# Performance work log

Measured on AMD Instinct MI355X. Metric: run time of the kernel, lower is better.

The kernel has to match this reference:

```python
import jax, jax.numpy as jnp
import numpy as np

HIDDEN = 2048
N_HEADS = 16
HEAD_DIM = 128
N_KV_HEADS = 4
MAX_POS = 4096
NEG_INF = -1e9


def _fixed_pos_embedding(features, length):
    # matches generate_fixed_pos_embedding: freqs over arange(0, features, 2)/features
    fraction = jnp.arange(0, features, 2, dtype=jnp.float32) / features
    timescale = 10000.0 ** fraction
    inv_freq = 1.0 / timescale
    sinusoid = jnp.einsum('i,j->ij', jnp.arange(length, dtype=jnp.float32), inv_freq)
    sinusoid = jnp.concatenate([sinusoid, sinusoid], axis=-1)  # [length, features]
    return jnp.sin(sinusoid), jnp.cos(sinusoid)


def setup_inputs() -> dict:
    key = jax.random.key(0)
    k0, k1, k2, k3, k4 = jax.random.split(key, 5)
    B, S = 2, 2048
    hidden_states = jax.random.normal(k0, (B, S, HIDDEN), dtype=jnp.float32)
    # causal additive mask [B,1,S,S]; module forces mask[:, :, :, 0] = 0
    causal = jnp.where(jnp.tril(jnp.ones((S, S), dtype=bool)), 0.0, NEG_INF).astype(jnp.float32)
    causal = causal.at[:, 0].set(0.0)
    attention_mask = jnp.broadcast_to(causal[None, None], (B, 1, S, S))
    std = 0.02
    q_w = jax.random.normal(k1, (N_HEADS * HEAD_DIM, HIDDEN), dtype=jnp.float32) * std
    k_w = jax.random.normal(k2, (N_KV_HEADS * HEAD_DIM, HIDDEN), dtype=jnp.float32) * std
    v_w = jax.random.normal(k3, (N_KV_HEADS * HEAD_DIM, HIDDEN), dtype=jnp.float32) * std
    o_w = jax.random.normal(k4, (HIDDEN, N_HEADS * HEAD_DIM), dtype=jnp.float32) * std
    sin, cos = _fixed_pos_embedding(HEAD_DIM, MAX_POS)
    return {"hidden_states": hidden_states, "attention_mask": attention_mask,
            "q_w": q_w, "k_w": k_w, "v_w": v_w, "o_w": o_w, "sin": sin, "cos": cos}


def _rotate_half(x):
    d = x.shape[-1] // 2
    return jnp.concatenate([-x[..., d:], x[..., :d]], axis=-1)


def reference(hidden_states, attention_mask, q_w, k_w, v_w, o_w, sin, cos):
    B, S, _ = hidden_states.shape
    D = cos.shape[-1]
    H = q_w.shape[0] // D
    KV = k_w.shape[0] // D
    n_rep = H // KV

    # QKV projections (nn.Linear: y = x @ W^T), split into heads: [B,S,h,D]
    q = jnp.einsum('bsh,oh->bso', hidden_states, q_w).reshape(B, S, H, D)
    k = jnp.einsum('bsh,oh->bso', hidden_states, k_w).reshape(B, S, KV, D)
    v = jnp.einsum('bsh,oh->bso', hidden_states, v_w).reshape(B, S, KV, D)

    # rotary embedding (non-decode path: q and k share cos/sin[:S])
    c = cos[:S][None, :, None, :]
    s = sin[:S][None, :, None, :]
    q = q * c + _rotate_half(q) * s
    k = k * c + _rotate_half(k) * s

    # repeat_kv (repeat_interleave along head dim) for GQA
    k = jnp.repeat(k, n_rep, axis=2)  # [B,S,H,D]
    v = jnp.repeat(v, n_rep, axis=2)

    # NOTE: no 1/sqrt(D) scaling -- module uses softmax_scale=1.0
    scores = jnp.einsum('bqhd,bkhd->bhqk', q, k) + attention_mask
    weights = jax.nn.softmax(scores.astype(jnp.float32), axis=-1).astype(q.dtype)
    attn = jnp.einsum('bhqk,bkhd->bqhd', weights, v).reshape(B, S, H * D)
    return jnp.einsum('bso,ho->bsh', attn, o_w)
```

## Files before the change

kernel.cpp:

```cpp
#include <hip/hip_runtime.h>

typedef __bf16 bf16x8 __attribute__((ext_vector_type(8)));
typedef float f32x4 __attribute__((ext_vector_type(4)));

#define LOG2E 1.44269504088896340736f

#define GLDS16(g, l) __builtin_amdgcn_global_load_lds(                         \
    (const __attribute__((address_space(1))) unsigned int*)(g),                \
    (__attribute__((address_space(3))) unsigned int*)(l), 16, 0, 0)

__global__ __launch_bounds__(256) void split_matrix(
    const float* __restrict__ src, __bf16* __restrict__ dh, __bf16* __restrict__ dl)
{
    const size_t t = (size_t)(blockIdx.x * 256 + threadIdx.x) * 8;
    float4 a = *(const float4*)(src + t);
    float4 b = *(const float4*)(src + t + 4);
    float f[8] = {a.x, a.y, a.z, a.w, b.x, b.y, b.z, b.w};
    bf16x8 h, l;
#pragma unroll
    for (int i = 0; i < 8; ++i) {
        __bf16 hh = (__bf16)f[i];
        h[i] = hh; l[i] = (__bf16)(f[i] - (float)hh);
    }
    *(bf16x8*)(dh + t) = h;
    *(bf16x8*)(dl + t) = l;
}

__global__ __launch_bounds__(256) void gemm_planes(
    const __bf16* __restrict__ Ah, const __bf16* __restrict__ Al,
    const __bf16* __restrict__ Bh, const __bf16* __restrict__ Bl,
    float* __restrict__ C, int K, int ldc)
{
    __shared__ __bf16 sAh[128 * 32], sAl[128 * 32];
    __shared__ __bf16 sBh[128 * 32], sBl[128 * 32];

    const int tid  = threadIdx.x;
    const int lane = tid & 63;
    const int wave = tid >> 6;
    const int m0 = blockIdx.y * 128;
    const int n0 = blockIdx.x * 128;

    const int sr  = wave * 32 + (lane >> 2);
    const int sc  = (lane & 3) * 8;
    const __bf16* ga0 = Ah + (size_t)(m0 + sr) * K + sc;
    const __bf16* ga1 = ga0 + (size_t)16 * K;
    const __bf16* gA0 = Al + (size_t)(m0 + sr) * K + sc;
    const __bf16* gA1 = gA0 + (size_t)16 * K;
    const __bf16* gb0 = Bh + (size_t)(n0 + sr) * K + sc;
    const __bf16* gb1 = gb0 + (size_t)16 * K;
    const __bf16* gB0 = Bl + (size_t)(n0 + sr) * K + sc;
    const __bf16* gB1 = gB0 + (size_t)16 * K;
    __bf16* la0 = &sAh[(wave * 32) * 32];
    __bf16* la1 = &sAh[(wave * 32 + 16) * 32];
    __bf16* lA0 = &sAl[(wave * 32) * 32];
    __bf16* lA1 = &sAl[(wave * 32 + 16) * 32];
    __bf16* lb0 = &sBh[(wave * 32) * 32];
    __bf16* lb1 = &sBh[(wave * 32 + 16) * 32];
    __bf16* lB0 = &sBl[(wave * 32) * 32];
    __bf16* lB1 = &sBl[(wave * 32 + 16) * 32];

    f32x4 acc[4][4];
    for (int mi = 0; mi < 4; ++mi)
        for (int ni = 0; ni < 4; ++ni)
            acc[mi][ni] = (f32x4){0.f, 0.f, 0.f, 0.f};

    const int wm = (wave & 1) * 64;
    const int wn = (wave >> 1) * 64;
    const int fr = lane & 15;
    const int fc = (lane >> 4) * 8;
    const int dr = (lane >> 4) * 4;

    for (int k0 = 0; k0 < K; k0 += 32) {
        GLDS16(ga0, la0); GLDS16(ga1, la1);
        GLDS16(gA0, lA0); GLDS16(gA1, lA1);
        GLDS16(gb0, lb0); GLDS16(gb1, lb1);
        GLDS16(gB0, lB0); GLDS16(gB1, lB1);
        ga0 += 32; ga1 += 32; gA0 += 32; gA1 += 32;
        gb0 += 32; gb1 += 32; gB0 += 32; gB1 += 32;
        __syncthreads();

        bf16x8 afh[4], afl[4], bfh[4], bfl[4];
#pragma unroll
        for (int i = 0; i < 4; ++i) {
            afh[i] = *(const bf16x8*)&sAh[(wm + i * 16 + fr) * 32 + fc];
            afl[i] = *(const bf16x8*)&sAl[(wm + i * 16 + fr) * 32 + fc];
            bfh[i] = *(const bf16x8*)&sBh[(wn + i * 16 + fr) * 32 + fc];
            bfl[i] = *(const bf16x8*)&sBl[(wn + i * 16 + fr) * 32 + fc];
        }
#pragma unroll
        for (int mi = 0; mi < 4; ++mi)
#pragma unroll
            for (int ni = 0; ni < 4; ++ni) {
                acc[mi][ni] = __builtin_amdgcn_mfma_f32_16x16x32_bf16(
                    afh[mi], bfh[ni], acc[mi][ni], 0, 0, 0);
                acc[mi][ni] = __builtin_amdgcn_mfma_f32_16x16x32_bf16(
                    afl[mi], bfh[ni], acc[mi][ni], 0, 0, 0);
                acc[mi][ni] = __builtin_amdgcn_mfma_f32_16x16x32_bf16(
                    afh[mi], bfl[ni], acc[mi][ni], 0, 0, 0);
            }
        __syncthreads();
    }

    for (int mi = 0; mi < 4; ++mi)
        for (int ni = 0; ni < 4; ++ni)
            for (int r = 0; r < 4; ++r) {
                int row = m0 + wm + mi * 16 + dr + r;
                int col = n0 + wn + ni * 16 + fr;
                C[(size_t)row * ldc + col] = acc[mi][ni][r];
            }
}

__global__ __launch_bounds__(256) void rope_q(
    float* __restrict__ qkv,
    const float* __restrict__ sinp, const float* __restrict__ cosp)
{
    int t = blockIdx.x * 256 + threadIdx.x;
    int row = t >> 10;
    int rem = t & 1023;
    int col = (rem >> 6) * 128 + (rem & 63);
    int s = row & 2047;
    int d = col & 127;

    float* p = qkv + (size_t)row * 3072 + col;
    float x0  = p[0];
    float x1  = p[64];
    float c0  = cosp[s * 128 + d];
    float c1  = cosp[s * 128 + d + 64];
    float sn0 = sinp[s * 128 + d];
    float sn1 = sinp[s * 128 + d + 64];
    p[0]  = x0 * c0 - x1 * sn0;
    p[64] = x1 * c1 + x0 * sn1;
}

__global__ __launch_bounds__(256) void prep_kv(
    const float* __restrict__ qkv,
    const float* __restrict__ sinp, const float* __restrict__ cosp,
    __bf16* __restrict__ ksp, __bf16* __restrict__ vtsp)
{
    __shared__ float vs[32][132];

    const int tid = threadIdx.x;
    const int kb  = blockIdx.x;
    const int kvh = blockIdx.y;
    const int b   = blockIdx.z;

    {
        const int key = tid >> 1;
        const int dh  = (tid & 1) * 32;
        const int pos = kb * 128 + key;
        const int ksw = key & 7;
        const float* src = qkv + (size_t)(b * 2048 + pos) * 3072 + 2048 + kvh * 128;
        __bf16* dst = ksp + ((size_t)((b * 4 + kvh) * 2048) + pos) * 256;
        const float* cp = cosp + pos * 128;
        const float* sp = sinp + pos * 128;
#pragma unroll
        for (int g = 0; g < 4; ++g) {
            int d0 = dh + g * 8;
            float4 x0a = *(const float4*)(src + d0);
            float4 x0b = *(const float4*)(src + d0 + 4);
            float4 x1a = *(const float4*)(src + d0 + 64);
            float4 x1b = *(const float4*)(src + d0 + 68);
            float4 c0a = *(const float4*)(cp + d0);
            float4 c0b = *(const float4*)(cp + d0 + 4);
            float4 c1a = *(const float4*)(cp + d0 + 64);
            float4 c1b = *(const float4*)(cp + d0 + 68);
            float4 s0a = *(const float4*)(sp + d0);
            float4 s0b = *(const float4*)(sp + d0 + 4);
            float4 s1a = *(const float4*)(sp + d0 + 64);
            float4 s1b = *(const float4*)(sp + d0 + 68);
            float x0[8] = {x0a.x,x0a.y,x0a.z,x0a.w,x0b.x,x0b.y,x0b.z,x0b.w};
            float x1[8] = {x1a.x,x1a.y,x1a.z,x1a.w,x1b.x,x1b.y,x1b.z,x1b.w};
            float c0[8] = {c0a.x,c0a.y,c0a.z,c0a.w,c0b.x,c0b.y,c0b.z,c0b.w};
            float c1[8] = {c1a.x,c1a.y,c1a.z,c1a.w,c1b.x,c1b.y,c1b.z,c1b.w};
            float s0[8] = {s0a.x,s0a.y,s0a.z,s0a.w,s0b.x,s0b.y,s0b.z,s0b.w};
            float s1[8] = {s1a.x,s1a.y,s1a.z,s1a.w,s1b.x,s1b.y,s1b.z,s1b.w};
            bf16x8 h0, l0, h1, l1;
#pragma unroll
            for (int i = 0; i < 8; ++i) {
                float y0 = x0[i] * c0[i] - x1[i] * s0[i];
                float y1 = x1[i] * c1[i] + x0[i] * s1[i];
                __bf16 hh0 = (__bf16)y0;
                __bf16 hh1 = (__bf16)y1;
                h0[i] = hh0; l0[i] = (__bf16)(y0 - (float)hh0);
                h1[i] = hh1; l1[i] = (__bf16)(y1 - (float)hh1);
            }
            const int bb = d0 >> 3;
            *(bf16x8*)(dst + ((bb        ^ ksw) << 3)) = h0;
            *(bf16x8*)(dst + (((bb + 8)  ^ ksw) << 3)) = h1;
            *(bf16x8*)(dst + (((bb + 16) ^ ksw) << 3)) = l0;
            *(bf16x8*)(dst + (((bb + 24) ^ ksw) << 3)) = l1;
        }
    }

    for (int st = 0; st < 4; ++st) {
        __syncthreads();
        {
            const int key = tid >> 3;
            const int dc  = (tid & 7) * 16;
            const float* vsrc = qkv + (size_t)(b * 2048 + kb * 128 + st * 32 + key) * 3072
                                + 2560 + kvh * 128 + dc;
            float4 v0 = *(const float4*)(vsrc);
            float4 v1 = *(const float4*)(vsrc + 4);
            float4 v2 = *(const float4*)(vsrc + 8);
            float4 v3 = *(const float4*)(vsrc + 12);
            *(float4*)&vs[key][dc]      = v0;
            *(float4*)&vs[key][dc + 4]  = v1;
            *(float4*)&vs[key][dc + 8]  = v2;
            *(float4*)&vs[key][dc + 12] = v3;
        }
        __syncthreads();
        {
            const int plane = tid >> 7;
            const int d     = tid & 127;
            bf16x8 ob[4];
#pragma unroll
            for (int k = 0; k < 32; ++k) {
                float x = vs[k][d];
                __bf16 hh = (__bf16)x;
                ob[k >> 3][k & 7] = plane ? (__bf16)(x - (float)hh) : hh;
            }
            const int rV  = plane * 128 + d;
            const int vsw = (d >> 1) & 3;
            __bf16* dst = vtsp + ((size_t)((b * 4 + kvh) * 64 + kb * 4 + st)) * 8192
                               + (size_t)rV * 32;
            *(bf16x8*)(dst + ((0 ^ vsw) << 3)) = ob[0];
            *(bf16x8*)(dst + ((1 ^ vsw) << 3)) = ob[1];
            *(bf16x8*)(dst + ((2 ^ vsw) << 3)) = ob[2];
            *(bf16x8*)(dst + ((3 ^ vsw) << 3)) = ob[3];
        }
    }
}

__global__ __launch_bounds__(256, 2) void flash_attn(
    const float* __restrict__ qkv,
    const __bf16* __restrict__ ksp,
    const __bf16* __restrict__ vtsp,
    __bf16* __restrict__ attnh, __bf16* __restrict__ attnl)
{
    __shared__ __bf16 Ks[2][32 * 256];
    __shared__ __bf16 Vt[2][256 * 32];
    __shared__ unsigned int Psf[4][2][512];

    const int tid  = threadIdx.x;
    const int lane = tid & 63;
    const int wave = tid >> 6;
    const int id   = blockIdx.x;
    const int pair = id & 7;
    const int kvh  = pair & 3;
    const int b    = pair >> 2;
    const int u    = id >> 3;
    const int qb   = (u >> 5) ? (u & 31) : 63 - (u & 31);
    const int h    = kvh * 4 + wave;

    const int fr  = lane & 15;
    const int g   = lane >> 4;
    const int fc  = g * 8;
    const int dr  = g * 4;
    const int frs = fr & 7;

    bf16x8 aqh[2][4], aql[2][4];
    for (int rs = 0; rs < 2; ++rs) {
        const size_t qrow = (size_t)(b * 2048 + qb * 32 + rs * 16 + fr) * 3072 + h * 128;
        for (int ks = 0; ks < 4; ++ks) {
            float4 qv[2];
            qv[0] = *(const float4*)(qkv + qrow + ks * 32 + fc);
            qv[1] = *(const float4*)(qkv + qrow + ks * 32 + fc + 4);
            const float* qf = (const float*)qv;
            bf16x8 h8, l8;
#pragma unroll
            for (int i = 0; i < 8; ++i) {
                float x = qf[i];
                __bf16 hh = (__bf16)x;
                h8[i] = hh; l8[i] = (__bf16)(x - (float)hh);
            }
            aqh[rs][ks] = h8; aql[rs][ks] = l8;
        }
    }
    asm volatile("s_waitcnt vmcnt(0)" ::: "memory");
    __builtin_amdgcn_sched_barrier(0);

    bf16x8 ones;
#pragma unroll
    for (int i = 0; i < 8; ++i) ones[i] = (__bf16)1.0f;

    f32x4 o[2][8];
    for (int rs = 0; rs < 2; ++rs)
        for (int dg = 0; dg < 8; ++dg) o[rs][dg] = (f32x4){0.f, 0.f, 0.f, 0.f};
    f32x4 ls[2] = {(f32x4){0.f,0.f,0.f,0.f}, (f32x4){0.f,0.f,0.f,0.f}};

    const int ntiles = qb + 1;
    const __bf16* kg0 = ksp + (size_t)(b * 4 + kvh) * 2048 * 256 + wave * 2048 + lane * 8;
    const __bf16* vg0 = vtsp + (size_t)(b * 4 + kvh) * 64 * 8192 + wave * 2048 + lane * 8;

    {
        __bf16* kl = &Ks[0][wave * 2048];
        __bf16* vl = &Vt[0][wave * 2048];
        GLDS16(kg0,        kl);       GLDS16(kg0 + 512,  kl + 512);
        GLDS16(kg0 + 1024, kl + 1024);GLDS16(kg0 + 1536, kl + 1536);
        GLDS16(vg0,        vl);       GLDS16(vg0 + 512,  vl + 512);
        GLDS16(vg0 + 1024, vl + 1024);GLDS16(vg0 + 1536, vl + 1536);
    }

    for (int kt = 0; kt < ntiles; ++kt) {
        if (kt + 1 < ntiles) {
            const __bf16* kg = kg0 + (size_t)(kt + 1) * 8192;
            const __bf16* vg = vg0 + (size_t)(kt + 1) * 8192;
            __bf16* kl = &Ks[(kt + 1) & 1][wave * 2048];
            __bf16* vl = &Vt[(kt + 1) & 1][wave * 2048];
            GLDS16(kg,        kl);       GLDS16(kg + 512,  kl + 512);
            GLDS16(kg + 1024, kl + 1024);GLDS16(kg + 1536, kl + 1536);
            GLDS16(vg,        vl);       GLDS16(vg + 512,  vl + 512);
            GLDS16(vg + 1024, vl + 1024);GLDS16(vg + 1536, vl + 1536);
            asm volatile("s_waitcnt vmcnt(8)" ::: "memory");
        } else {
            asm volatile("s_waitcnt vmcnt(0)" ::: "memory");
        }
        __builtin_amdgcn_sched_barrier(0);
        __builtin_amdgcn_s_barrier();
        __builtin_amdgcn_sched_barrier(0);

        const int buf = kt & 1;
        const int k0 = kt * 32;

        f32x4 s[2][2];
        s[0][0] = s[0][1] = s[1][0] = s[1][1] = (f32x4){0.f, 0.f, 0.f, 0.f};
        __builtin_amdgcn_s_setprio(1);
#pragma unroll
        for (int ks = 0; ks < 4; ++ks) {
            const int bh = ks * 4 + g;
            bf16x8 b0h = *(const bf16x8*)&Ks[buf][fr * 256        + ((bh        ^ frs) << 3)];
            bf16x8 b0l = *(const bf16x8*)&Ks[buf][fr * 256        + (((bh + 16) ^ frs) << 3)];
            bf16x8 b1h = *(const bf16x8*)&Ks[buf][(16 + fr) * 256 + ((bh        ^ frs) << 3)];
            bf16x8 b1l = *(const bf16x8*)&Ks[buf][(16 + fr) * 256 + (((bh + 16) ^ frs) << 3)];
#pragma unroll
            for (int rs = 0; rs < 2; ++rs) {
                s[rs][0] = __builtin_amdgcn_mfma_f32_16x16x32_bf16(aqh[rs][ks], b0h, s[rs][0], 0, 0, 0);
                s[rs][0] = __builtin_amdgcn_mfma_f32_16x16x32_bf16(aql[rs][ks], b0h, s[rs][0], 0, 0, 0);
                s[rs][0] = __builtin_amdgcn_mfma_f32_16x16x32_bf16(aqh[rs][ks], b0l, s[rs][0], 0, 0, 0);
                s[rs][1] = __builtin_amdgcn_mfma_f32_16x16x32_bf16(aqh[rs][ks], b1h, s[rs][1], 0, 0, 0);
                s[rs][1] = __builtin_amdgcn_mfma_f32_16x16x32_bf16(aql[rs][ks], b1h, s[rs][1], 0, 0, 0);
                s[rs][1] = __builtin_amdgcn_mfma_f32_16x16x32_bf16(aqh[rs][ks], b1l, s[rs][1], 0, 0, 0);
            }
        }
        __builtin_amdgcn_s_setprio(0);

        const bool diag = (kt == ntiles - 1);
#pragma unroll
        for (int rs = 0; rs < 2; ++rs) {
            f32x4 s0 = s[rs][0], s1 = s[rs][1];
            if (diag) {
#pragma unroll
                for (int r = 0; r < 4; ++r) {
                    const int qg = qb * 32 + rs * 16 + dr + r;
                    if (k0 + fr > qg)      s0[r] = -1e30f;
                    if (k0 + 16 + fr > qg) s1[r] = -1e30f;
                }
            }
            uint4 w0, w1;
#pragma unroll
            for (int r = 0; r < 4; ++r) {
                float x0 = exp2f(s0[r] * LOG2E);
                float x1 = exp2f(s1[r] * LOG2E);
                __bf16 h0 = (__bf16)x0;
                __bf16 h1 = (__bf16)x1;
                unsigned u0 = ((unsigned)__builtin_bit_cast(unsigned short, h0) << 16)
                            |  (unsigned)__builtin_bit_cast(unsigned short, (__bf16)(x0 - (float)h0));
                unsigned u1 = ((unsigned)__builtin_bit_cast(unsigned short, h1) << 16)
                            |  (unsigned)__builtin_bit_cast(unsigned short, (__bf16)(x1 - (float)h1));
                ((unsigned*)&w0)[r] = u0;
                ((unsigned*)&w1)[r] = u1;
            }
            unsigned int* pw = &Psf[wave][rs][0];
            const int sb = (fr * 4 + g) ^ (((fr >> 3) & 1) << 2);
            *(uint4*)(pw + sb * 4)        = w0;
            *(uint4*)(pw + (sb + 64) * 4) = w1;
        }
        asm volatile("s_waitcnt lgkmcnt(0)" ::: "memory");
        __builtin_amdgcn_sched_barrier(0);

        bf16x8 ph[2], pl[2];
#pragma unroll
        for (int rs = 0; rs < 2; ++rs) {
#pragma unroll
            for (int j = 0; j < 8; ++j) {
                const int col = fc + j;
                const int sR  = (col * 4 + (fr >> 2)) ^ ((g & 1) << 2);
                const unsigned v = Psf[wave][rs][sR * 4 + (fr & 3)];
                ph[rs][j] = __builtin_bit_cast(__bf16, (unsigned short)(v >> 16));
                pl[rs][j] = __builtin_bit_cast(__bf16, (unsigned short)(v & 0xffffu));
            }
        }

        __builtin_amdgcn_s_setprio(1);
        ls[0] = __builtin_amdgcn_mfma_f32_16x16x32_bf16(ph[0], ones, ls[0], 0, 0, 0);
        ls[0] = __builtin_amdgcn_mfma_f32_16x16x32_bf16(pl[0], ones, ls[0], 0, 0, 0);
        ls[1] = __builtin_amdgcn_mfma_f32_16x16x32_bf16(ph[1], ones, ls[1], 0, 0, 0);
        ls[1] = __builtin_amdgcn_mfma_f32_16x16x32_bf16(pl[1], ones, ls[1], 0, 0, 0);
#pragma unroll
        for (int dg = 0; dg < 8; ++dg) {
            const int d0 = dg * 16 + fr;
            const int sw = (g ^ ((d0 >> 1) & 3)) << 3;
            bf16x8 bvh = *(const bf16x8*)&Vt[buf][d0 * 32 + sw];
            bf16x8 bvl = *(const bf16x8*)&Vt[buf][(d0 + 128) * 32 + sw];
#pragma unroll
            for (int rs = 0; rs < 2; ++rs) {
                o[rs][dg] = __builtin_amdgcn_mfma_f32_16x16x32_bf16(ph[rs], bvh, o[rs][dg], 0, 0, 0);
                o[rs][dg] = __builtin_amdgcn_mfma_f32_16x16x32_bf16(pl[rs], bvh, o[rs][dg], 0, 0, 0);
                o[rs][dg] = __builtin_amdgcn_mfma_f32_16x16x32_bf16(ph[rs], bvl, o[rs][dg], 0, 0, 0);
            }
        }
        __builtin_amdgcn_s_setprio(0);

        __builtin_amdgcn_s_barrier();
    }

    for (int rs = 0; rs < 2; ++rs) {
        const size_t orow = (size_t)(b * 2048 + qb * 32 + rs * 16);
        for (int dg = 0; dg < 8; ++dg)
            for (int r = 0; r < 4; ++r) {
                float val = o[rs][dg][r] / ls[rs][r];
                size_t idx = (orow + dr + r) * 2048 + h * 128 + dg * 16 + fr;
                __bf16 hh = (__bf16)val;
                attnh[idx] = hh;
                attnl[idx] = (__bf16)(val - (float)hh);
            }
    }
}

extern "C" void kernel_launch(void* const* d_in, const int* in_sizes, int n_in,
                              void* d_out, int out_size, void* d_ws, size_t ws_size,
                              hipStream_t stream)
{
    const float* hs   = (const float*)d_in[0];
    const float* qw   = (const float*)d_in[2];
    const float* kw   = (const float*)d_in[3];
    const float* vw   = (const float*)d_in[4];
    const float* ow   = (const float*)d_in[5];
    const float* sinp = (const float*)d_in[6];
    const float* cosp = (const float*)d_in[7];
    float* outp = (float*)d_out;

    char* w = (char*)d_ws;
    float*  qkv  = (float*)w;   w += (size_t)4096 * 3072 * 4;
    __bf16* ksp  = (__bf16*)w;  w += (size_t)8 * 2048 * 256 * 2;
    __bf16* vtsp = (__bf16*)w;  w += (size_t)8 * 64 * 8192 * 2;
    __bf16* wqh  = (__bf16*)w;  w += (size_t)3072 * 2048 * 2;
    __bf16* wql  = (__bf16*)w;  w += (size_t)3072 * 2048 * 2;
    __bf16* owh  = (__bf16*)w;  w += (size_t)2048 * 2048 * 2;
    __bf16* owl  = (__bf16*)w;  w += (size_t)2048 * 2048 * 2;
    __bf16* hsh  = (__bf16*)w;  w += (size_t)4096 * 2048 * 2;
    __bf16* hsl  = (__bf16*)w;  w += (size_t)4096 * 2048 * 2;
    __bf16* attnh = hsh;
    __bf16* attnl = hsl;

    split_matrix<<<4096, 256, 0, stream>>>(hs, hsh, hsl);
    split_matrix<<<2048, 256, 0, stream>>>(qw, wqh, wql);
    split_matrix<<<512,  256, 0, stream>>>(kw, wqh + (size_t)2048 * 2048,
                                               wql + (size_t)2048 * 2048);
    split_matrix<<<512,  256, 0, stream>>>(vw, wqh + (size_t)2560 * 2048,
                                               wql + (size_t)2560 * 2048);
    split_matrix<<<2048, 256, 0, stream>>>(ow, owh, owl);

    gemm_planes<<<dim3(24, 32), 256, 0, stream>>>(hsh, hsl, wqh, wql, qkv, 2048, 3072);
    rope_q<<<16384, 256, 0, stream>>>(qkv, sinp, cosp);
    prep_kv<<<dim3(16, 4, 2), 256, 0, stream>>>(qkv, sinp, cosp, ksp, vtsp);
    flash_attn<<<512, 256, 0, stream>>>(qkv, ksp, vtsp, attnh, attnl);
    gemm_planes<<<dim3(16, 32), 256, 0, stream>>>(attnh, attnl, owh, owl, outp, 2048, 2048);
}
```

Measured before the change: 600.5 us.

## Rewrite split-bf16 GEMM with larger tiles, double buffering and swizzled LDS layout

Replaces the 128x128 single-buffered GEMM with a 512-thread kernel that uses 256xBN tiles (192 for QKV, 128 for output projection), double-buffered LDS staging via global_load_lds and explicit vmcnt waits, and a remapped block order for cache locality. The split and attention-output writers now store bf16 planes in an XOR-swizzled layout so LDS fragment reads avoid bank conflicts. This targets the projection GEMMs' load latency and LDS conflicts. In exchange it adds register pressure, hardcodes K=2048 and grid shapes, and ties the layout of all producers to the new reader.

```diff
diff --git a/kernel.cpp b/kernel.cpp
--- a/kernel.cpp
+++ b/kernel.cpp
@@ -8,6 +8,7 @@
 #define GLDS16(g, l) __builtin_amdgcn_global_load_lds(                         \
     (const __attribute__((address_space(1))) unsigned int*)(g),                \
     (__attribute__((address_space(3))) unsigned int*)(l), 16, 0, 0)
+
 
 __global__ __launch_bounds__(256) void split_matrix(
     const float* __restrict__ src, __bf16* __restrict__ dh, __bf16* __restrict__ dl)
@@ -22,92 +23,153 @@
         __bf16 hh = (__bf16)f[i];
         h[i] = hh; l[i] = (__bf16)(f[i] - (float)hh);
     }
-    *(bf16x8*)(dh + t) = h;
-    *(bf16x8*)(dl + t) = l;
+    const int r  = (int)(t >> 11);
+    const int sw = (r ^ (r >> 2)) & 3;
+    const size_t d = (t & ~(size_t)31) + ((size_t)((((int)(t >> 3) & 3) ^ sw)) << 3);
+    *(bf16x8*)(dh + d) = h;
+    *(bf16x8*)(dl + d) = l;
 }
 
-__global__ __launch_bounds__(256) void gemm_planes(
+template<int BN, int NLOAD>
+__global__ __launch_bounds__(512, 2) void gemm_planes8(
     const __bf16* __restrict__ Ah, const __bf16* __restrict__ Al,
     const __bf16* __restrict__ Bh, const __bf16* __restrict__ Bl,
-    float* __restrict__ C, int K, int ldc)
+    float* __restrict__ C, int ldc)
 {
-    __shared__ __bf16 sAh[128 * 32], sAl[128 * 32];
-    __shared__ __bf16 sBh[128 * 32], sBl[128 * 32];
+    constexpr int WN = BN / 4;
+    constexpr int NF = WN / 16;
+
+    __shared__ __bf16 sAh[2][256 * 32];
+    __shared__ __bf16 sAl[2][256 * 32];
+    __shared__ __bf16 sBh[2][BN * 32];
+    __shared__ __bf16 sBl[2][BN * 32];
 
     const int tid  = threadIdx.x;
     const int lane = tid & 63;
     const int wave = tid >> 6;
-    const int m0 = blockIdx.y * 128;
-    const int n0 = blockIdx.x * 128;
-
-    const int sr  = wave * 32 + (lane >> 2);
-    const int sc  = (lane & 3) * 8;
-    const __bf16* ga0 = Ah + (size_t)(m0 + sr) * K + sc;
-    const __bf16* ga1 = ga0 + (size_t)16 * K;
-    const __bf16* gA0 = Al + (size_t)(m0 + sr) * K + sc;
-    const __bf16* gA1 = gA0 + (size_t)16 * K;
-    const __bf16* gb0 = Bh + (size_t)(n0 + sr) * K + sc;
-    const __bf16* gb1 = gb0 + (size_t)16 * K;
-    const __bf16* gB0 = Bl + (size_t)(n0 + sr) * K + sc;
-    const __bf16* gB1 = gB0 + (size_t)16 * K;
-    __bf16* la0 = &sAh[(wave * 32) * 32];
-    __bf16* la1 = &sAh[(wave * 32 + 16) * 32];
-    __bf16* lA0 = &sAl[(wave * 32) * 32];
-    __bf16* lA1 = &sAl[(wave * 32 + 16) * 32];
-    __bf16* lb0 = &sBh[(wave * 32) * 32];
-    __bf16* lb1 = &sBh[(wave * 32 + 16) * 32];
-    __bf16* lB0 = &sBl[(wave * 32) * 32];
-    __bf16* lB1 = &sBl[(wave * 32 + 16) * 32];
-
-    f32x4 acc[4][4];
-    for (int mi = 0; mi < 4; ++mi)
-        for (int ni = 0; ni < 4; ++ni)
-            acc[mi][ni] = (f32x4){0.f, 0.f, 0.f, 0.f};
-
-    const int wm = (wave & 1) * 64;
-    const int wn = (wave >> 1) * 64;
-    const int fr = lane & 15;
-    const int fc = (lane >> 4) * 8;
-    const int dr = (lane >> 4) * 4;
-
-    for (int k0 = 0; k0 < K; k0 += 32) {
-        GLDS16(ga0, la0); GLDS16(ga1, la1);
-        GLDS16(gA0, lA0); GLDS16(gA1, lA1);
-        GLDS16(gb0, lb0); GLDS16(gb1, lb1);
-        GLDS16(gB0, lB0); GLDS16(gB1, lB1);
-        ga0 += 32; ga1 += 32; gA0 += 32; gA1 += 32;
-        gb0 += 32; gb1 += 32; gB0 += 32; gB1 += 32;
-        __syncthreads();
-
-        bf16x8 afh[4], afl[4], bfh[4], bfl[4];
-#pragma unroll
-        for (int i = 0; i < 4; ++i) {
-            afh[i] = *(const bf16x8*)&sAh[(wm + i * 16 + fr) * 32 + fc];
-            afl[i] = *(const bf16x8*)&sAl[(wm + i * 16 + fr) * 32 + fc];
-            bfh[i] = *(const bf16x8*)&sBh[(wn + i * 16 + fr) * 32 + fc];
-            bfl[i] = *(const bf16x8*)&sBl[(wn + i * 16 + fr) * 32 + fc];
-        }
-#pragma unroll
-        for (int mi = 0; mi < 4; ++mi)
-#pragma unroll
-            for (int ni = 0; ni < 4; ++ni) {
-                acc[mi][ni] = __builtin_amdgcn_mfma_f32_16x16x32_bf16(
-                    afh[mi], bfh[ni], acc[mi][ni], 0, 0, 0);
-                acc[mi][ni] = __builtin_amdgcn_mfma_f32_16x16x32_bf16(
-                    afl[mi], bfh[ni], acc[mi][ni], 0, 0, 0);
-                acc[mi][ni] = __builtin_amdgcn_mfma_f32_16x16x32_bf16(
-                    afh[mi], bfl[ni], acc[mi][ni], 0, 0, 0);
-            }
-        __syncthreads();
-    }
-
-    for (int mi = 0; mi < 4; ++mi)
-        for (int ni = 0; ni < 4; ++ni)
-            for (int r = 0; r < 4; ++r) {
-                int row = m0 + wm + mi * 16 + dr + r;
-                int col = n0 + wn + ni * 16 + fr;
-                C[(size_t)row * ldc + col] = acc[mi][ni][r];
-            }
+    const int wm   = (wave & 1) * 128;
+    const int wn   = (wave >> 1) * WN;
+
+    const int idg = blockIdx.y * 16 + blockIdx.x;
+    const int swb = (idg & 7) * 32 + (idg >> 3);
+    const int m0  = (swb >> 4) * 256;
+    const int n0  = (swb & 15) * BN;
+
+    const int fr  = lane & 15;
+    const int g   = lane >> 4;
+    const int dr  = g * 4;
+    const int sxr = (fr ^ (fr >> 2)) & 3;
+    const int pA  = (g ^ sxr) << 3;
+
+    const int srow = tid >> 2;
+    const int spb  = (tid & 3) << 3;
+    const __bf16* gAh0 = Ah + (size_t)(m0 + srow) * 2048 + spb;
+    const __bf16* gAh1 = gAh0 + (size_t)128 * 2048;
+    const __bf16* gAl0 = Al + (size_t)(m0 + srow) * 2048 + spb;
+    const __bf16* gAl1 = gAl0 + (size_t)128 * 2048;
+    const __bf16* gBh0 = Bh + (size_t)(n0 + srow) * 2048 + spb;
+    const __bf16* gBl0 = Bl + (size_t)(n0 + srow) * 2048 + spb;
+    const __bf16* gX5  = Bl;
+    const __bf16* gBl6 = Bl;
+    if constexpr (BN == 192) {
+        gX5 = (tid < 256)
+            ? Bh + (size_t)(n0 + 128 + srow) * 2048 + spb
+            : Bl + (size_t)(n0 + ((tid - 256) >> 2)) * 2048 + (((tid - 256) & 3) << 3);
+        gBl6 = Bl + (size_t)(n0 + 64 + srow) * 2048 + spb;
+    }
+
+#define STAGE8(bb)                                                             \
+    do {                                                                       \
+        GLDS16(gAh0, &sAh[bb][tid * 8]);                                       \
+        GLDS16(gAh1, &sAh[bb][4096 + tid * 8]);                                \
+        GLDS16(gAl0, &sAl[bb][tid * 8]);                                       \
+        GLDS16(gAl1, &sAl[bb][4096 + tid * 8]);                                \
+        GLDS16(gBh0, &sBh[bb][tid * 8]);                                       \
+        if constexpr (BN == 192) {                                             \
+            if (tid < 256) { GLDS16(gX5, &sBh[bb][4096 + tid * 8]); }          \
+            else           { GLDS16(gX5, &sBl[bb][(tid - 256) * 8]); }         \
+            GLDS16(gBl6, &sBl[bb][2048 + tid * 8]);                            \
+        } else {                                                               \
+            GLDS16(gBl0, &sBl[bb][tid * 8]);                                   \
+        }                                                                      \
+    } while (0)
+
+#define ADV8()                                                                 \
+    do {                                                                       \
+        gAh0 += 32; gAh1 += 32; gAl0 += 32; gAl1 += 32;                        \
+        gBh0 += 32; gBl0 += 32;                                                \
+        if constexpr (BN == 192) { gX5 += 32; gBl6 += 32; }                    \
+    } while (0)
+
+    f32x4 acc[8][NF];
+#pragma unroll
+    for (int mf = 0; mf < 8; ++mf)
+#pragma unroll
+        for (int nf = 0; nf < NF; ++nf)
+            acc[mf][nf] = (f32x4){0.f, 0.f, 0.f, 0.f};
+
+    STAGE8(0);
+    ADV8();
+
+    for (int t = 0; t < 64; ++t) {
+        const int buf = t & 1;
+        if (t < 63) {
+            STAGE8(buf ^ 1);
+            ADV8();
+            __builtin_amdgcn_sched_barrier(0);
+            if constexpr (NLOAD == 7) asm volatile("s_waitcnt vmcnt(7)" ::: "memory");
+            else                      asm volatile("s_waitcnt vmcnt(6)" ::: "memory");
+        } else {
+            __builtin_amdgcn_sched_barrier(0);
+            asm volatile("s_waitcnt vmcnt(0)" ::: "memory");
+        }
+        __builtin_amdgcn_sched_barrier(0);
+        __builtin_amdgcn_s_barrier();
+        __builtin_amdgcn_sched_barrier(0);
+
+        bf16x8 bh[NF], bl[NF];
+#pragma unroll
+        for (int p = 0; p < 4; ++p) {
+            if (p == 0) {
+#pragma unroll
+                for (int nf = 0; nf < NF; ++nf) {
+                    bh[nf] = *(const bf16x8*)&sBh[buf][(wn + nf * 16 + fr) * 32 + pA];
+                    bl[nf] = *(const bf16x8*)&sBl[buf][(wn + nf * 16 + fr) * 32 + pA];
+                }
+            }
+            bf16x8 a0h = *(const bf16x8*)&sAh[buf][(wm + p * 32 + fr) * 32 + pA];
+            bf16x8 a0l = *(const bf16x8*)&sAl[buf][(wm + p * 32 + fr) * 32 + pA];
+            bf16x8 a1h = *(const bf16x8*)&sAh[buf][(wm + p * 32 + 16 + fr) * 32 + pA];
+            bf16x8 a1l = *(const bf16x8*)&sAl[buf][(wm + p * 32 + 16 + fr) * 32 + pA];
+            __builtin_amdgcn_sched_barrier(0);
+            __builtin_amdgcn_s_barrier();
+            __builtin_amdgcn_sched_barrier(0);
+            __builtin_amdgcn_s_setprio(1);
+#pragma unroll
+            for (int nf = 0; nf < NF; ++nf) {
+                acc[2 * p][nf] = __builtin_amdgcn_mfma_f32_16x16x32_bf16(a0h, bh[nf], acc[2 * p][nf], 0, 0, 0);
+                acc[2 * p][nf] = __builtin_amdgcn_mfma_f32_16x16x32_bf16(a0l, bh[nf], acc[2 * p][nf], 0, 0, 0);
+                acc[2 * p][nf] = __builtin_amdgcn_mfma_f32_16x16x32_bf16(a0h, bl[nf], acc[2 * p][nf], 0, 0, 0);
+                acc[2 * p + 1][nf] = __builtin_amdgcn_mfma_f32_16x16x32_bf16(a1h, bh[nf], acc[2 * p + 1][nf], 0, 0, 0);
+                acc[2 * p + 1][nf] = __builtin_amdgcn_mfma_f32_16x16x32_bf16(a1l, bh[nf], acc[2 * p + 1][nf], 0, 0, 0);
+                acc[2 * p + 1][nf] = __builtin_amdgcn_mfma_f32_16x16x32_bf16(a1h, bl[nf], acc[2 * p + 1][nf], 0, 0, 0);
+            }
+            __builtin_amdgcn_s_setprio(0);
+        }
+    }
+
+#pragma unroll
+    for (int mf = 0; mf < 8; ++mf)
+#pragma unroll
+        for (int nf = 0; nf < NF; ++nf)
+#pragma unroll
+            for (int rr = 0; rr < 4; ++rr) {
+                const int row = m0 + wm + mf * 16 + dr + rr;
+                const int col = n0 + wn + nf * 16 + fr;
+                C[(size_t)row * ldc + col] = acc[mf][nf][rr];
+            }
+#undef STAGE8
+#undef ADV8
 }
 
 __global__ __launch_bounds__(256) void rope_q(
@@ -419,7 +481,11 @@
         for (int dg = 0; dg < 8; ++dg)
             for (int r = 0; r < 4; ++r) {
                 float val = o[rs][dg][r] / ls[rs][r];
-                size_t idx = (orow + dr + r) * 2048 + h * 128 + dg * 16 + fr;
+                const int rl  = dr + r;
+                const int swz = (rl ^ (rl >> 2)) & 3;
+                const int col = h * 128 + dg * 16 + fr;
+                const size_t idx = (size_t)(orow + rl) * 2048 + (col & ~31)
+                                 + ((((col >> 3) & 3) ^ swz) << 3) + (col & 7);
                 __bf16 hh = (__bf16)val;
                 attnh[idx] = hh;
                 attnl[idx] = (__bf16)(val - (float)hh);
@@ -461,9 +527,9 @@
                                                wql + (size_t)2560 * 2048);
     split_matrix<<<2048, 256, 0, stream>>>(ow, owh, owl);
 
-    gemm_planes<<<dim3(24, 32), 256, 0, stream>>>(hsh, hsl, wqh, wql, qkv, 2048, 3072);
+    gemm_planes8<192, 7><<<dim3(16, 16), 512, 0, stream>>>(hsh, hsl, wqh, wql, qkv, 3072);
     rope_q<<<16384, 256, 0, stream>>>(qkv, sinp, cosp);
     prep_kv<<<dim3(16, 4, 2), 256, 0, stream>>>(qkv, sinp, cosp, ksp, vtsp);
     flash_attn<<<512, 256, 0, stream>>>(qkv, ksp, vtsp, attnh, attnl);
-    gemm_planes<<<dim3(16, 32), 256, 0, stream>>>(attnh, attnl, owh, owl, outp, 2048, 2048);
+    gemm_planes8<128, 6><<<dim3(16, 16), 512, 0, stream>>>(attnh, attnl, owh, owl, outp, 2048);
 }
```

New measurement: 587.3 us. -2.2%, faster.
